# Optimization experiments

Measured on AMD Instinct MI355X. Metric: run time of the kernel, lower is better.

## Reference

```python
import jax, jax.numpy as jnp
import numpy as np

NUM_NODES = 100000
NUM_EDGES = 1600000
HID = 128
NODE_DIM = 5
MSG_DIM = 2


def _mlp(x, params):
    # 3 hidden ReLU layers + linear head, matching nn.Sequential in torch
    (W0, b0, W1, b1, W2, b2, W3, b3) = params
    h = jax.nn.relu(x @ W0 + b0)
    h = jax.nn.relu(h @ W1 + b1)
    h = jax.nn.relu(h @ W2 + b2)
    return h @ W3 + b3


def setup_inputs() -> dict:
    key = jax.random.key(0)
    ks = jax.random.split(key, 12)
    nodes = jax.random.normal(ks[0], (NUM_NODES, NODE_DIM), dtype=jnp.float32)
    edge_index = jax.random.randint(ks[1], (2, NUM_EDGES), 0, NUM_NODES, dtype=jnp.int32)

    def lin(k, fan_in, fan_out):
        # kaiming-uniform-ish init, scale irrelevant for correctness baseline
        bound = 1.0 / np.sqrt(fan_in)
        return jax.random.uniform(k, (fan_in, fan_out), jnp.float32, -bound, bound)

    return {
        "nodes": nodes,
        "edge_index": edge_index,
        "Wm0": lin(ks[2], 2 * NODE_DIM, HID), "bm0": jnp.zeros((HID,), jnp.float32),
        "Wm1": lin(ks[3], HID, HID),          "bm1": jnp.zeros((HID,), jnp.float32),
        "Wm2": lin(ks[4], HID, HID),          "bm2": jnp.zeros((HID,), jnp.float32),
        "Wm3": lin(ks[5], HID, MSG_DIM),      "bm3": jnp.zeros((MSG_DIM,), jnp.float32),
        "Wu0": lin(ks[6], NODE_DIM + MSG_DIM, HID), "bu0": jnp.zeros((HID,), jnp.float32),
        "Wu1": lin(ks[7], HID, HID),          "bu1": jnp.zeros((HID,), jnp.float32),
        "Wu2": lin(ks[8], HID, HID),          "bu2": jnp.zeros((HID,), jnp.float32),
        "Wu3": lin(ks[9], HID, MSG_DIM),      "bu3": jnp.zeros((MSG_DIM,), jnp.float32),
    }


def reference(nodes, edge_index, Wm0, bm0, Wm1, bm1, Wm2, bm2, Wm3, bm3,
              Wu0, bu0, Wu1, bu1, Wu2, bu2, Wu3, bu3):
    senders = edge_index[0]
    receivers = edge_index[1]
    # gather endpoints: [E, 2*node_dim]
    edge_inputs = jnp.concatenate([nodes[senders], nodes[receivers]], axis=-1)
    messages = _mlp(edge_inputs, (Wm0, bm0, Wm1, bm1, Wm2, bm2, Wm3, bm3))  # [E, msg_dim]
    # scatter-add pooling rho_{e->v}
    pooled = jax.ops.segment_sum(messages, receivers, num_segments=nodes.shape[0])  # [N, msg_dim]
    node_update_input = jnp.concatenate([nodes, pooled], axis=-1)  # [N, node_dim+msg_dim]
    delta_v = _mlp(node_update_input, (Wu0, bu0, Wu1, bu1, Wu2, bu2, Wu3, bu3))  # [N, 2]
    # Euler step on velocity columns 2:4
    updated = jnp.concatenate([nodes[:, :2], nodes[:, 2:4] + delta_v, nodes[:, 4:]], axis=-1)
    return updated
```

## Files before the change

kernel.cpp:

```cpp
#include <hip/hip_runtime.h>
#include <hip/hip_bf16.h>

#define NE 1600000
#define NN 100000
#define PSCALE 131072.0f

typedef __attribute__((ext_vector_type(8))) short s16x8;
typedef __attribute__((ext_vector_type(4))) float f32x4;
typedef __attribute__((ext_vector_type(16))) float f32x16;
typedef __attribute__((ext_vector_type(4))) uint u32x4;

__device__ __forceinline__ ushort f2b(float v) {
  union { __hip_bfloat16 h; ushort u; } c; c.h = __float2bfloat16(v); return c.u;
}
__device__ __forceinline__ uint cvtpk(float a, float b) {
  uint r;
  asm("v_cvt_pk_bf16_f32 %0, %1, %2" : "=v"(r) : "v"(a), "v"(b));
  return r;
}
__device__ __forceinline__ uint pkrelu(float a, float b) {
  a = fmaxf(a, 0.f); b = fmaxf(b, 0.f);
  return cvtpk(a, b);
}
__device__ __forceinline__ f32x16 mfma32(s16x8 a, s16x8 b, f32x16 c) {
  return __builtin_amdgcn_mfma_f32_32x32x16_bf16(a, b, c, 0, 0, 0);
}
__device__ __forceinline__ u32x4 packg(const f32x16& a, int g) {
  u32x4 r;
#pragma unroll
  for (int w = 0; w < 4; w++) r[w] = pkrelu(a[8 * g + 2 * w], a[8 * g + 2 * w + 1]);
  return r;
}
__device__ __forceinline__ f32x16 loadbias(const float* bias, int mt, int hi) {
  f32x16 b;
#pragma unroll
  for (int q4 = 0; q4 < 4; q4++) {
    f32x4 v = *(const f32x4*)(bias + mt * 32 + q4 * 8 + hi * 4);
#pragma unroll
    for (int i = 0; i < 4; i++) b[q4 * 4 + i] = v[i];
  }
  return b;
}

__global__ void prep_weights(const float* s0, const float* s1, const float* s2, const float* s3,
                             const float* s4, const float* s5, const float* s6, const float* s7,
                             const float* bm0, const float* bu0, ushort* dst) {
  const int NFRAG[8] = {4, 32, 32, 8, 4, 32, 32, 8};
  const int offs[8]  = {0, 2048, 18432, 34816, 38912, 40960, 57344, 73728};
  const float* srcs[8] = {s0, s1, s2, s3, s4, s5, s6, s7};
  int b = blockIdx.x;
  int cnt = NFRAG[b] * 512;
  const float* src = srcs[b];
  bool isProducer = (b == 0 || b == 4);
  bool isHead = (b == 3 || b == 7);
  int F1 = (b < 4) ? 5 : 2;
  int kbias = (b < 4) ? 13 : 10;
  const float* bp = (b < 4) ? bm0 : bu0;
  ushort* d = dst + offs[b];
  for (int idx = threadIdx.x; idx < cnt; idx += blockDim.x) {
    int f = idx >> 9, r = idx & 511, lane = r >> 3, j = r & 7;
    int hi = lane >> 5, m = lane & 31;
    float v = 0.f;
    if (isProducer) {
      int ch = f * 32 + m;
      int k = hi * 8 + j;
      int row = -1;
      if (k < 5) row = k;
      else if (k >= 8 && k < 8 + F1) row = k - 3;
      if (row >= 0) v = src[row * 128 + ch];
      else if (k == kbias) v = bp[ch];
    } else {
      int s = isHead ? f : (f >> 2);
      int k = s * 16 + hi * 8 + j;
      int c = (k & ~12) | ((k & 4) << 1) | ((k & 8) >> 1);
      if (isHead) v = (m < 2) ? src[c * 2 + m] : 0.f;
      else {
        int ch = (f & 3) * 32 + m;
        v = src[c * 128 + ch];
      }
    }
    d[idx] = f2b(v);
  }
}

template <int MODE>
__global__ __launch_bounds__(512, 2)
void gnn_kernel(const float* __restrict__ nodes,
                const int* __restrict__ eidx,
                unsigned long long* __restrict__ pooled,
                const ushort* __restrict__ wsrc,
                const float* __restrict__ b1g, const float* __restrict__ b2g,
                const float* __restrict__ b3g,
                float* __restrict__ out) {
  __shared__ __align__(16) char hand[65536];
  __shared__ __align__(16) float bias1[128];
  __shared__ __align__(16) float bias2[128];
  __shared__ __align__(16) float bias3[16];
  __shared__ uint flags[64];
  if (threadIdx.x < 128) {
    bias1[threadIdx.x] = b1g[threadIdx.x];
    bias2[threadIdx.x] = b2g[threadIdx.x];
  }
  if (threadIdx.x < 16) bias3[threadIdx.x] = (threadIdx.x < 2) ? b3g[threadIdx.x] : 0.f;
  if (threadIdx.x < 64) flags[threadIdx.x] = 0u;

  const int wv = threadIdx.x >> 6;
  const int l = threadIdx.x & 63;
  const int hi = l >> 5;
  const int e32 = l & 31;
  const bool front = (wv < 4);
  const int pr = wv & 3;
  char* hbase = hand + pr * 16384;
  volatile uint* prodv = &flags[pr * 8];
  volatile uint* consv = &flags[32 + pr * 8];

  s16x8 WA[8];
  s16x8 WB[8][4];
  if (front) {
#pragma unroll
    for (int mt = 0; mt < 4; mt++)
      WA[mt] = *(const s16x8*)(wsrc + ((mt * 64 + l) * 8));
#pragma unroll
    for (int s = 0; s < 8; s++)
#pragma unroll
      for (int mt = 0; mt < 4; mt++)
        WB[s][mt] = *(const s16x8*)(wsrc + 2048 + (((s * 4 + mt) * 64 + l) * 8));
  } else {
#pragma unroll
    for (int s = 0; s < 8; s++)
      WA[s] = *(const s16x8*)(wsrc + 34816 + ((s * 64 + l) * 8));
#pragma unroll
    for (int s = 0; s < 8; s++)
#pragma unroll
      for (int mt = 0; mt < 4; mt++)
        WB[s][mt] = *(const s16x8*)(wsrc + 18432 + (((s * 4 + mt) * 64 + l) * 8));
  }
  __syncthreads();

  const int np = gridDim.x << 2;
  const int gp = (blockIdx.x << 2) + pr;
  const int NB = (MODE == 0) ? (NE / 32) : (NN / 32);
  const f32x16 z16 = {0.f, 0.f, 0.f, 0.f, 0.f, 0.f, 0.f, 0.f,
                      0.f, 0.f, 0.f, 0.f, 0.f, 0.f, 0.f, 0.f};

  if (front) {
    float g0 = 0, g1 = 0, g2 = 0, g3 = 0, g4 = 0;
    auto PREF = [&](int bb) {
      if (bb < NB) {
        int e = (bb << 5) + e32;
        if (MODE == 0) {
          int idx = eidx[hi * NE + e];
          const float* np_ = nodes + idx * 5;
          g0 = np_[0]; g1 = np_[1]; g2 = np_[2]; g3 = np_[3]; g4 = np_[4];
        } else {
          if (hi == 0) {
            const float* np_ = nodes + e * 5;
            g0 = np_[0]; g1 = np_[1]; g2 = np_[2]; g3 = np_[3]; g4 = np_[4];
          } else {
            unsigned long long pl = pooled[e];
            int x32 = (int)(uint)pl;
            int y32 = (int)(pl >> 32) + (x32 < 0 ? 1 : 0);
            g0 = (float)x32 * (1.f / PSCALE);
            g1 = (float)y32 * (1.f / PSCALE);
          }
        }
      }
    };
    PREF(gp);

    int t = 0;
#pragma unroll 1
    for (int b = gp; b < NB; b += np, ++t) {
      s16x8 xf;
      {
        u32x4 f = {0u, 0u, 0u, 0u};
        if (MODE == 0) {
          f[0] = cvtpk(g0, g1); f[1] = cvtpk(g2, g3);
          f[2] = cvtpk(g4, hi ? 1.0f : 0.0f);
        } else {
          if (hi == 0) { f[0] = cvtpk(g0, g1); f[1] = cvtpk(g2, g3); f[2] = cvtpk(g4, 0.f); }
          else         { f[0] = cvtpk(g0, g1); f[1] = cvtpk(1.0f, 0.f); }
        }
        xf = __builtin_bit_cast(s16x8, f);
      }
      PREF(b + np);

      u32x4 phA[4][2];
#pragma unroll
      for (int mt = 0; mt < 4; mt++) {
        f32x16 a = mfma32(WA[mt], xf, z16);
        phA[mt][0] = packg(a, 0);
        phA[mt][1] = packg(a, 1);
      }
      if (t >= 2) {
        while (*consv < (uint)(t - 1)) __builtin_amdgcn_s_sleep(1);
        __builtin_amdgcn_sched_barrier(0);
      }
      char* wb = hbase + (t & 1) * 8192;
#pragma unroll
      for (int mt = 0; mt < 4; mt++) {
        f32x16 a = mfma32(WB[0][mt], __builtin_bit_cast(s16x8, phA[0][0]),
                          loadbias(bias1, mt, hi));
#pragma unroll
        for (int s = 1; s < 8; s++)
          a = mfma32(WB[s][mt], __builtin_bit_cast(s16x8, phA[s >> 1][s & 1]), a);
        u32x4 h0 = packg(a, 0), h1 = packg(a, 1);
        *(u32x4*)(wb + ((mt << 1) + 0) * 1024 + l * 16) = h0;
        *(u32x4*)(wb + ((mt << 1) + 1) * 1024 + l * 16) = h1;
      }
      __builtin_amdgcn_sched_barrier(0);
      if (l == 0) *prodv = (uint)(t + 1);
      __builtin_amdgcn_sched_barrier(0);
    }
  } else {
    int bc = 0;
#pragma unroll 1
    for (int b = gp; b < NB; b += np, ++bc) {
      const int rbase = b << 5;
      int rc = 0;
      if (MODE == 0 && hi == 0) rc = eidx[NE + rbase + e32];
      while (*prodv < (uint)(bc + 1)) __builtin_amdgcn_s_sleep(1);
      __builtin_amdgcn_sched_barrier(0);
      const char* rb = hbase + (bc & 1) * 8192;
      u32x4 pin[8];
#pragma unroll
      for (int s = 0; s < 8; s++)
        pin[s] = *(const u32x4*)(rb + s * 1024 + l * 16);
      __builtin_amdgcn_sched_barrier(0);
      if (l == 0) *consv = (uint)(bc + 1);
      __builtin_amdgcn_sched_barrier(0);
      u32x4 phC[4][2];
#pragma unroll
      for (int mt = 0; mt < 4; mt++) {
        f32x16 a = mfma32(WB[0][mt], __builtin_bit_cast(s16x8, pin[0]),
                          loadbias(bias2, mt, hi));
#pragma unroll
        for (int s = 1; s < 8; s++)
          a = mfma32(WB[s][mt], __builtin_bit_cast(s16x8, pin[s]), a);
        phC[mt][0] = packg(a, 0);
        phC[mt][1] = packg(a, 1);
      }
      f32x16 a = mfma32(WA[0], __builtin_bit_cast(s16x8, phC[0][0]), z16);
#pragma unroll
      for (int s = 1; s < 8; s++)
        a = mfma32(WA[s], __builtin_bit_cast(s16x8, phC[s >> 1][s & 1]), a);

      int e = rbase + e32;
      if (hi == 0) {
        float mv0 = a[0] + bias3[0], mv1 = a[1] + bias3[1];
        if (MODE == 0) {
          int ix = (int)rintf(mv0 * PSCALE);
          int iy = (int)rintf(mv1 * PSCALE);
          long long ad = (((long long)iy) << 32) + (long long)ix;
          atomicAdd(&pooled[rc], (unsigned long long)ad);
        } else {
          out[e * 5 + 2] = nodes[e * 5 + 2] + mv0;
          out[e * 5 + 3] = nodes[e * 5 + 3] + mv1;
        }
      } else if (MODE == 1) {
        out[e * 5 + 0] = nodes[e * 5 + 0];
        out[e * 5 + 1] = nodes[e * 5 + 1];
        out[e * 5 + 4] = nodes[e * 5 + 4];
      }
    }
  }
}

extern "C" void kernel_launch(void* const* d_in, const int* in_sizes, int n_in,
                              void* d_out, int out_size, void* d_ws, size_t ws_size,
                              hipStream_t stream) {
  const float* nodes = (const float*)d_in[0];
  const int* eidx = (const int*)d_in[1];
  const float* Wm0 = (const float*)d_in[2];  const float* bm0 = (const float*)d_in[3];
  const float* Wm1 = (const float*)d_in[4];  const float* bm1 = (const float*)d_in[5];
  const float* Wm2 = (const float*)d_in[6];  const float* bm2 = (const float*)d_in[7];
  const float* Wm3 = (const float*)d_in[8];  const float* bm3 = (const float*)d_in[9];
  const float* Wu0 = (const float*)d_in[10]; const float* bu0 = (const float*)d_in[11];
  const float* Wu1 = (const float*)d_in[12]; const float* bu1 = (const float*)d_in[13];
  const float* Wu2 = (const float*)d_in[14]; const float* bu2 = (const float*)d_in[15];
  const float* Wu3 = (const float*)d_in[16]; const float* bu3 = (const float*)d_in[17];

  unsigned long long* pooled = (unsigned long long*)d_ws;
  ushort* wbuf = (ushort*)((char*)d_ws + 800000);

  hipMemsetAsync(pooled, 0, NN * 8, stream);
  prep_weights<<<8, 256, 0, stream>>>(Wm0, Wm1, Wm2, Wm3, Wu0, Wu1, Wu2, Wu3,
                                      bm0, bu0, wbuf);

  gnn_kernel<0><<<256, 512, 0, stream>>>(nodes, eidx, pooled, wbuf,
                                         bm1, bm2, bm3, nullptr);
  gnn_kernel<1><<<256, 512, 0, stream>>>(nodes, nullptr, pooled, wbuf + 38912,
                                         bu1, bu2, bu3, (float*)d_out);
}
```

Before: 170.4 us.

## Replace producer/consumer wave split with per-wave full MLP using LDS-staged weights

Removes the front/back wave specialization, where front waves computed layers 0-1 and handed activations through LDS with spin-wait flags to back waves computing layers 2-3. Every wave now runs the whole MLP for its own 32-row block, streaming weight fragments from an LDS copy of all weights with double-buffered register prefetch. This drops the inter-wave handoff, the flag polling and the register-resident weight split, and doubles the number of waves working on independent blocks. In exchange each MFMA now needs weight fragments read from LDS, which adds LDS bandwidth pressure and latency.

```diff
diff --git a/kernel.cpp b/kernel.cpp
--- a/kernel.cpp
+++ b/kernel.cpp
@@ -8,6 +8,7 @@
 typedef __attribute__((ext_vector_type(8))) short s16x8;
 typedef __attribute__((ext_vector_type(4))) float f32x4;
 typedef __attribute__((ext_vector_type(16))) float f32x16;
+typedef __attribute__((ext_vector_type(4))) int i32x4;
 typedef __attribute__((ext_vector_type(4))) uint u32x4;
 
 __device__ __forceinline__ ushort f2b(float v) {
@@ -92,176 +93,147 @@
                 const float* __restrict__ b1g, const float* __restrict__ b2g,
                 const float* __restrict__ b3g,
                 float* __restrict__ out) {
-  __shared__ __align__(16) char hand[65536];
+  __shared__ __align__(16) ushort wlds[38912];
   __shared__ __align__(16) float bias1[128];
   __shared__ __align__(16) float bias2[128];
   __shared__ __align__(16) float bias3[16];
-  __shared__ uint flags[64];
-  if (threadIdx.x < 128) {
-    bias1[threadIdx.x] = b1g[threadIdx.x];
-    bias2[threadIdx.x] = b2g[threadIdx.x];
-  }
-  if (threadIdx.x < 16) bias3[threadIdx.x] = (threadIdx.x < 2) ? b3g[threadIdx.x] : 0.f;
-  if (threadIdx.x < 64) flags[threadIdx.x] = 0u;
+  {
+    i32x4* dw = (i32x4*)wlds;
+    const i32x4* sw = (const i32x4*)wsrc;
+    for (int i = threadIdx.x; i < 4864; i += 512) dw[i] = sw[i];
+    if (threadIdx.x < 128) {
+      bias1[threadIdx.x] = b1g[threadIdx.x];
+      bias2[threadIdx.x] = b2g[threadIdx.x];
+    }
+    if (threadIdx.x < 16) bias3[threadIdx.x] = (threadIdx.x < 2) ? b3g[threadIdx.x] : 0.f;
+  }
+  __syncthreads();
 
   const int wv = threadIdx.x >> 6;
   const int l = threadIdx.x & 63;
   const int hi = l >> 5;
   const int e32 = l & 31;
-  const bool front = (wv < 4);
-  const int pr = wv & 3;
-  char* hbase = hand + pr * 16384;
-  volatile uint* prodv = &flags[pr * 8];
-  volatile uint* consv = &flags[32 + pr * 8];
-
-  s16x8 WA[8];
-  s16x8 WB[8][4];
-  if (front) {
-#pragma unroll
-    for (int mt = 0; mt < 4; mt++)
-      WA[mt] = *(const s16x8*)(wsrc + ((mt * 64 + l) * 8));
-#pragma unroll
-    for (int s = 0; s < 8; s++)
-#pragma unroll
-      for (int mt = 0; mt < 4; mt++)
-        WB[s][mt] = *(const s16x8*)(wsrc + 2048 + (((s * 4 + mt) * 64 + l) * 8));
-  } else {
-#pragma unroll
-    for (int s = 0; s < 8; s++)
-      WA[s] = *(const s16x8*)(wsrc + 34816 + ((s * 64 + l) * 8));
-#pragma unroll
-    for (int s = 0; s < 8; s++)
-#pragma unroll
-      for (int mt = 0; mt < 4; mt++)
-        WB[s][mt] = *(const s16x8*)(wsrc + 18432 + (((s * 4 + mt) * 64 + l) * 8));
-  }
-  __syncthreads();
-
-  const int np = gridDim.x << 2;
-  const int gp = (blockIdx.x << 2) + pr;
+  auto LF = [&](int base, int f) {
+    return *(const s16x8*)(wlds + base + f * 512 + l * 8);
+  };
+
+  int wid = blockIdx.x * 8 + wv;
+  int nwv = gridDim.x * 8;
   const int NB = (MODE == 0) ? (NE / 32) : (NN / 32);
   const f32x16 z16 = {0.f, 0.f, 0.f, 0.f, 0.f, 0.f, 0.f, 0.f,
                       0.f, 0.f, 0.f, 0.f, 0.f, 0.f, 0.f, 0.f};
 
-  if (front) {
-    float g0 = 0, g1 = 0, g2 = 0, g3 = 0, g4 = 0;
-    auto PREF = [&](int bb) {
-      if (bb < NB) {
-        int e = (bb << 5) + e32;
-        if (MODE == 0) {
-          int idx = eidx[hi * NE + e];
-          const float* np_ = nodes + idx * 5;
+  float g0 = 0, g1 = 0, g2 = 0, g3 = 0, g4 = 0;
+  auto PREF = [&](int bb) {
+    if (bb < NB) {
+      int e = (bb << 5) + e32;
+      if (MODE == 0) {
+        int idx = eidx[hi * NE + e];
+        const float* np_ = nodes + idx * 5;
+        g0 = np_[0]; g1 = np_[1]; g2 = np_[2]; g3 = np_[3]; g4 = np_[4];
+      } else {
+        if (hi == 0) {
+          const float* np_ = nodes + e * 5;
           g0 = np_[0]; g1 = np_[1]; g2 = np_[2]; g3 = np_[3]; g4 = np_[4];
         } else {
-          if (hi == 0) {
-            const float* np_ = nodes + e * 5;
-            g0 = np_[0]; g1 = np_[1]; g2 = np_[2]; g3 = np_[3]; g4 = np_[4];
-          } else {
-            unsigned long long pl = pooled[e];
-            int x32 = (int)(uint)pl;
-            int y32 = (int)(pl >> 32) + (x32 < 0 ? 1 : 0);
-            g0 = (float)x32 * (1.f / PSCALE);
-            g1 = (float)y32 * (1.f / PSCALE);
-          }
+          unsigned long long pl = pooled[e];
+          int x32 = (int)(uint)pl;
+          int y32 = (int)(pl >> 32) + (x32 < 0 ? 1 : 0);
+          g0 = (float)x32 * (1.f / PSCALE);
+          g1 = (float)y32 * (1.f / PSCALE);
         }
       }
-    };
-    PREF(gp);
-
-    int t = 0;
+    }
+  };
+  PREF(wid);
+
 #pragma unroll 1
-    for (int b = gp; b < NB; b += np, ++t) {
-      s16x8 xf;
-      {
-        u32x4 f = {0u, 0u, 0u, 0u};
-        if (MODE == 0) {
-          f[0] = cvtpk(g0, g1); f[1] = cvtpk(g2, g3);
-          f[2] = cvtpk(g4, hi ? 1.0f : 0.0f);
-        } else {
-          if (hi == 0) { f[0] = cvtpk(g0, g1); f[1] = cvtpk(g2, g3); f[2] = cvtpk(g4, 0.f); }
-          else         { f[0] = cvtpk(g0, g1); f[1] = cvtpk(1.0f, 0.f); }
-        }
-        xf = __builtin_bit_cast(s16x8, f);
-      }
-      PREF(b + np);
-
-      u32x4 phA[4][2];
-#pragma unroll
-      for (int mt = 0; mt < 4; mt++) {
-        f32x16 a = mfma32(WA[mt], xf, z16);
-        phA[mt][0] = packg(a, 0);
-        phA[mt][1] = packg(a, 1);
-      }
-      if (t >= 2) {
-        while (*consv < (uint)(t - 1)) __builtin_amdgcn_s_sleep(1);
-        __builtin_amdgcn_sched_barrier(0);
-      }
-      char* wb = hbase + (t & 1) * 8192;
-#pragma unroll
-      for (int mt = 0; mt < 4; mt++) {
-        f32x16 a = mfma32(WB[0][mt], __builtin_bit_cast(s16x8, phA[0][0]),
-                          loadbias(bias1, mt, hi));
-#pragma unroll
-        for (int s = 1; s < 8; s++)
-          a = mfma32(WB[s][mt], __builtin_bit_cast(s16x8, phA[s >> 1][s & 1]), a);
-        u32x4 h0 = packg(a, 0), h1 = packg(a, 1);
-        *(u32x4*)(wb + ((mt << 1) + 0) * 1024 + l * 16) = h0;
-        *(u32x4*)(wb + ((mt << 1) + 1) * 1024 + l * 16) = h1;
-      }
-      __builtin_amdgcn_sched_barrier(0);
-      if (l == 0) *prodv = (uint)(t + 1);
-      __builtin_amdgcn_sched_barrier(0);
-    }
-  } else {
-    int bc = 0;
-#pragma unroll 1
-    for (int b = gp; b < NB; b += np, ++bc) {
-      const int rbase = b << 5;
-      int rc = 0;
-      if (MODE == 0 && hi == 0) rc = eidx[NE + rbase + e32];
-      while (*prodv < (uint)(bc + 1)) __builtin_amdgcn_s_sleep(1);
-      __builtin_amdgcn_sched_barrier(0);
-      const char* rb = hbase + (bc & 1) * 8192;
-      u32x4 pin[8];
+  for (int b = wid; b < NB; b += nwv) {
+    const int rbase = b << 5;
+    int rc = 0;
+    if (MODE == 0) rc = eidx[NE + rbase + e32];
+    s16x8 xf;
+    {
+      u32x4 f = {0u, 0u, 0u, 0u};
+      if (MODE == 0) {
+        f[0] = cvtpk(g0, g1); f[1] = cvtpk(g2, g3);
+        f[2] = cvtpk(g4, hi ? 1.0f : 0.0f);
+      } else {
+        if (hi == 0) { f[0] = cvtpk(g0, g1); f[1] = cvtpk(g2, g3); f[2] = cvtpk(g4, 0.f); }
+        else         { f[0] = cvtpk(g0, g1); f[1] = cvtpk(1.0f, 0.f); }
+      }
+      xf = __builtin_bit_cast(s16x8, f);
+    }
+    PREF(b + nwv);
+
+    s16x8 w0f0 = LF(0, 0), w0f1 = LF(0, 1), w0f2 = LF(0, 2), w0f3 = LF(0, 3);
+    s16x8 wf[2][8];
+#pragma unroll
+    for (int s = 0; s < 8; s++) wf[0][s] = LF(2048, s * 4);
+
+    u32x4 phA[4][2];
+    {
+      f32x16 a;
+      a = mfma32(w0f0, xf, z16); phA[0][0] = packg(a, 0); phA[0][1] = packg(a, 1);
+      a = mfma32(w0f1, xf, z16); phA[1][0] = packg(a, 0); phA[1][1] = packg(a, 1);
+      a = mfma32(w0f2, xf, z16); phA[2][0] = packg(a, 0); phA[2][1] = packg(a, 1);
+      a = mfma32(w0f3, xf, z16); phA[3][0] = packg(a, 0); phA[3][1] = packg(a, 1);
+    }
+    u32x4 phB[4][2];
+#pragma unroll
+    for (int mt = 0; mt < 4; mt++) {
+      if (mt < 3) {
+#pragma unroll
+        for (int s = 0; s < 8; s++) wf[(mt + 1) & 1][s] = LF(2048, s * 4 + mt + 1);
+      } else {
+#pragma unroll
+        for (int s = 0; s < 8; s++) wf[(mt + 1) & 1][s] = LF(18432, s * 4);
+      }
+      f32x16 a = loadbias(bias1, mt, hi);
 #pragma unroll
       for (int s = 0; s < 8; s++)
-        pin[s] = *(const u32x4*)(rb + s * 1024 + l * 16);
-      __builtin_amdgcn_sched_barrier(0);
-      if (l == 0) *consv = (uint)(bc + 1);
-      __builtin_amdgcn_sched_barrier(0);
-      u32x4 phC[4][2];
-#pragma unroll
-      for (int mt = 0; mt < 4; mt++) {
-        f32x16 a = mfma32(WB[0][mt], __builtin_bit_cast(s16x8, pin[0]),
-                          loadbias(bias2, mt, hi));
-#pragma unroll
-        for (int s = 1; s < 8; s++)
-          a = mfma32(WB[s][mt], __builtin_bit_cast(s16x8, pin[s]), a);
-        phC[mt][0] = packg(a, 0);
-        phC[mt][1] = packg(a, 1);
-      }
-      f32x16 a = mfma32(WA[0], __builtin_bit_cast(s16x8, phC[0][0]), z16);
-#pragma unroll
-      for (int s = 1; s < 8; s++)
-        a = mfma32(WA[s], __builtin_bit_cast(s16x8, phC[s >> 1][s & 1]), a);
-
-      int e = rbase + e32;
-      if (hi == 0) {
-        float mv0 = a[0] + bias3[0], mv1 = a[1] + bias3[1];
-        if (MODE == 0) {
-          int ix = (int)rintf(mv0 * PSCALE);
-          int iy = (int)rintf(mv1 * PSCALE);
-          long long ad = (((long long)iy) << 32) + (long long)ix;
-          atomicAdd(&pooled[rc], (unsigned long long)ad);
-        } else {
-          out[e * 5 + 2] = nodes[e * 5 + 2] + mv0;
-          out[e * 5 + 3] = nodes[e * 5 + 3] + mv1;
-        }
-      } else if (MODE == 1) {
-        out[e * 5 + 0] = nodes[e * 5 + 0];
-        out[e * 5 + 1] = nodes[e * 5 + 1];
-        out[e * 5 + 4] = nodes[e * 5 + 4];
-      }
+        a = mfma32(wf[mt & 1][s], __builtin_bit_cast(s16x8, phA[s >> 1][s & 1]), a);
+      phB[mt][0] = packg(a, 0);
+      phB[mt][1] = packg(a, 1);
+    }
+    u32x4 phC[4][2];
+#pragma unroll
+    for (int mt = 0; mt < 4; mt++) {
+      if (mt < 3) {
+#pragma unroll
+        for (int s = 0; s < 8; s++) wf[(mt + 1) & 1][s] = LF(18432, s * 4 + mt + 1);
+      } else {
+#pragma unroll
+        for (int s = 0; s < 8; s++) wf[(mt + 1) & 1][s] = LF(34816, s);
+      }
+      f32x16 a = loadbias(bias2, mt, hi);
+#pragma unroll
+      for (int s = 0; s < 8; s++)
+        a = mfma32(wf[mt & 1][s], __builtin_bit_cast(s16x8, phB[s >> 1][s & 1]), a);
+      phC[mt][0] = packg(a, 0);
+      phC[mt][1] = packg(a, 1);
+    }
+    f32x16 a = mfma32(wf[0][0], __builtin_bit_cast(s16x8, phC[0][0]), z16);
+#pragma unroll
+    for (int s = 1; s < 8; s++)
+      a = mfma32(wf[0][s], __builtin_bit_cast(s16x8, phC[s >> 1][s & 1]), a);
+
+    int e = rbase + e32;
+    if (hi == 0) {
+      float mv0 = a[0] + bias3[0], mv1 = a[1] + bias3[1];
+      if (MODE == 0) {
+        int ix = (int)rintf(mv0 * PSCALE);
+        int iy = (int)rintf(mv1 * PSCALE);
+        long long ad = (((long long)iy) << 32) + (long long)ix;
+        atomicAdd(&pooled[rc], (unsigned long long)ad);
+      } else {
+        out[e * 5 + 2] = nodes[e * 5 + 2] + mv0;
+        out[e * 5 + 3] = nodes[e * 5 + 3] + mv1;
+      }
+    } else if (MODE == 1) {
+      out[e * 5 + 0] = nodes[e * 5 + 0];
+      out[e * 5 + 1] = nodes[e * 5 + 1];
+      out[e * 5 + 4] = nodes[e * 5 + 4];
     }
   }
 }
```

New measurement: 165.9 us. 2.7% less time.
